# Kernel tuning notes

Measured on AMD Instinct MI355X. Metric: run time of the kernel, lower is better.

Reference implementation:

```python
import jax, jax.numpy as jnp
import numpy as np

DIM = 384
KERNEL = 31
PAD = KERNEL // 2


def setup_inputs() -> dict:
    key = jax.random.key(0)
    k1, k2 = jax.random.split(key)
    x = jax.random.normal(k1, (32, DIM, 56, 56), dtype=jnp.float32)
    weight = jax.random.normal(k2, (DIM, 1, KERNEL, KERNEL), dtype=jnp.float32)
    bias_term = jnp.zeros((DIM,), dtype=jnp.float32)
    return {"x": x, "weight": weight, "bias_term": bias_term}


def reference(x, weight, bias_term):
    # Depthwise conv2d: groups == channels, stride 1, SAME-style padding k//2.
    out = jax.lax.conv_general_dilated(
        x, weight,
        window_strides=(1, 1),
        padding=[(PAD, PAD), (PAD, PAD)],
        dimension_numbers=("NCHW", "OIHW", "NCHW"),
        feature_group_count=DIM,
    )
    return out + bias_term[None, :, None, None]
```

## Files before the change

### kernel.cpp

```cpp
#include <hip/hip_runtime.h>


#define DIMC 384
#define HW 56
#define KS 31
#define PADK 15
#define TROWS 86
#define TCOLS 88
#define RH 14
#define NP 16

typedef _Float16 half2v __attribute__((ext_vector_type(2)));

__device__ __forceinline__ float dot2f(half2v a, half2v b, float c) {
#if defined(__has_builtin) && __has_builtin(__builtin_amdgcn_fdot2)
    return __builtin_amdgcn_fdot2(a, b, c, false);
#else
    return fmaf((float)a.x, (float)b.x, fmaf((float)a.y, (float)b.y, c));
#endif
}

__global__ __launch_bounds__(256, 4)
void dwconv31_dot2(const float* __restrict__ x,
                   const float* __restrict__ w,
                   const float* __restrict__ bias,
                   float* __restrict__ out)
{
    __shared__ _Float16 t0[TROWS * TCOLS];
    __shared__ _Float16 t1[TROWS * TCOLS];
    __shared__ half2v  wlds[KS * NP];

    const int plane = blockIdx.x;
    const int c = plane % DIMC;
    const float* __restrict__ xp = x + (size_t)plane * (HW * HW);
    const float* __restrict__ wp = w + (size_t)c * (KS * KS);
    const int tid = threadIdx.x;

    for (int i = tid; i < KS * NP; i += 256) {
        int kh = i / NP, p = i - kh * NP;
        float a = wp[kh * KS + 2 * p];
        float b = (2 * p + 1 < KS) ? wp[kh * KS + 2 * p + 1] : 0.0f;
        half2v hv;
        hv.x = (_Float16)a;
        hv.y = (_Float16)b;
        wlds[i] = hv;
    }

    for (int idx = tid; idx < TROWS * TCOLS; idx += 256) {
        int r  = idx / TCOLS;
        int cc = idx - r * TCOLS;
        int gr = r - PADK;
        int gc = cc - PADK;
        float v = 0.0f;
        if ((unsigned)gr < (unsigned)HW && (unsigned)gc < (unsigned)HW)
            v = xp[gr * HW + gc];
        _Float16 hv = (_Float16)v;
        t0[r * TCOLS + cc] = hv;
        if (cc >= 1) t1[r * TCOLS + cc - 1] = hv;
        else         t1[r * TCOLS + TCOLS - 1] = (_Float16)0.0f;
    }
    __syncthreads();

    const int tx = tid & 63;
    const int h0 = (tid >> 6) * RH;

    float acc[RH];
#pragma unroll
    for (int j = 0; j < RH; ++j) acc[j] = 0.0f;

    if (tx < HW) {
        const _Float16* base = (tx & 1) ? (t1 + (tx - 1)) : (t0 + tx);

#pragma unroll 1
        for (int p = 0; p < NP; ++p) {
            const _Float16* colp = base + 2 * p;
#pragma unroll 1
            for (int khc = 0; khc < 2; ++khc) {
                const int kh0 = khc * 16;
                const int nkh = khc ? 15 : 16;

                half2v xr[29];
#pragma unroll
                for (int i = 0; i < 29; ++i)
                    xr[i] = *(const half2v*)(colp + (h0 + kh0 + i) * TCOLS);

#pragma unroll
                for (int kk = 0; kk < 16; ++kk) {
                    if (kk < nkh) {
                        half2v wv = wlds[(kh0 + kk) * NP + p];
#pragma unroll
                        for (int j = 0; j < RH; ++j)
                            acc[j] = dot2f(xr[kk + j], wv, acc[j]);
                    }
                }
            }
        }

        const float b = bias[c];
        float* __restrict__ op = out + (size_t)plane * (HW * HW);
#pragma unroll
        for (int j = 0; j < RH; ++j)
            op[(h0 + j) * HW + tx] = acc[j] + b;
    }
}

extern "C" void kernel_launch(void* const* d_in, const int* in_sizes, int n_in,
                              void* d_out, int out_size, void* d_ws, size_t ws_size,
                              hipStream_t stream) {
    const float* x    = (const float*)d_in[0];
    const float* wgt  = (const float*)d_in[1];
    const float* bias = (const float*)d_in[2];
    float* out = (float*)d_out;

    const int nplanes = 32 * DIMC;
    dwconv31_dot2<<<nplanes, 256, 0, stream>>>(x, wgt, bias, out);
}
```

Measured before the change: 908.7 us.

## Transpose LDS tile to column-major and pair vertical taps for dot2

```diff
diff --git a/kernel.cpp b/kernel.cpp
--- a/kernel.cpp
+++ b/kernel.cpp
@@ -1,16 +1,17 @@
 #include <hip/hip_runtime.h>
+#include <stdint.h>
 
 
 #define DIMC 384
 #define HW 56
 #define KS 31
-#define PADK 15
-#define TROWS 86
-#define TCOLS 88
-#define RH 14
-#define NP 16
+#define RH 28
+#define NM 16
+#define TW 86
+#define TH 88
 
 typedef _Float16 half2v __attribute__((ext_vector_type(2)));
+typedef _Float16 half8v __attribute__((ext_vector_type(8)));
 
 __device__ __forceinline__ float dot2f(half2v a, half2v b, float c) {
 #if defined(__has_builtin) && __has_builtin(__builtin_amdgcn_fdot2)
@@ -20,83 +21,100 @@
 #endif
 }
 
-__global__ __launch_bounds__(256, 4)
-void dwconv31_dot2(const float* __restrict__ x,
-                   const float* __restrict__ w,
-                   const float* __restrict__ bias,
-                   float* __restrict__ out)
+template<int G>
+__device__ __forceinline__ void conv_cols(const _Float16* __restrict__ tile,
+                                          const half2v* __restrict__ wlds,
+                                          int tx, float* __restrict__ acc)
 {
-    __shared__ _Float16 t0[TROWS * TCOLS];
-    __shared__ _Float16 t1[TROWS * TCOLS];
-    __shared__ half2v  wlds[KS * NP];
+    constexpr int P0 = 14 * G;
+    constexpr int AG = P0 & ~3;
+    constexpr int DG = P0 - AG;
+
+#pragma unroll 1
+    for (int kw = 0; kw < KS; ++kw) {
+        const int col = tx + kw;
+        const char* cbase = (const char*)tile + col * (TH * 2) + AG * 4;
+
+        half2v X[32];
+#pragma unroll
+        for (int q = 0; q < 8; ++q) {
+            half8v r = *(const half8v*)(cbase + 16 * q);
+            X[4 * q + 0] = __builtin_shufflevector(r, r, 0, 1);
+            X[4 * q + 1] = __builtin_shufflevector(r, r, 2, 3);
+            X[4 * q + 2] = __builtin_shufflevector(r, r, 4, 5);
+            X[4 * q + 3] = __builtin_shufflevector(r, r, 6, 7);
+        }
+
+        half2v Wt[32];
+        const char* wbase = (const char*)wlds + (kw << 7);
+#pragma unroll
+        for (int q = 0; q < 8; ++q) {
+            half8v r = *(const half8v*)(wbase + 16 * q);
+            Wt[4 * q + 0] = __builtin_shufflevector(r, r, 0, 1);
+            Wt[4 * q + 1] = __builtin_shufflevector(r, r, 2, 3);
+            Wt[4 * q + 2] = __builtin_shufflevector(r, r, 4, 5);
+            Wt[4 * q + 3] = __builtin_shufflevector(r, r, 6, 7);
+        }
+
+#pragma unroll
+        for (int j = 0; j < RH; ++j) {
+            const int off = DG + ((j + (j & 1)) >> 1);
+            const int ws  = (j & 1) ? 0 : 16;
+#pragma unroll
+            for (int m = 0; m < NM; ++m)
+                acc[j] = dot2f(X[off + m], Wt[ws + m], acc[j]);
+        }
+    }
+}
+
+__global__ __launch_bounds__(128, 4)
+void dwconv31_v5(const float* __restrict__ x, const float* __restrict__ w,
+                 const float* __restrict__ bias, float* __restrict__ out)
+{
+    __shared__ __align__(16) _Float16 tile[TW * TH];
+    __shared__ __align__(16) half2v  wlds[KS * 32];
 
     const int plane = blockIdx.x;
     const int c = plane % DIMC;
     const float* __restrict__ xp = x + (size_t)plane * (HW * HW);
-    const float* __restrict__ wp = w + (size_t)c * (KS * KS);
+    const float* __restrict__ wc = w + (size_t)c * (KS * KS);
     const int tid = threadIdx.x;
 
-    for (int i = tid; i < KS * NP; i += 256) {
-        int kh = i / NP, p = i - kh * NP;
-        float a = wp[kh * KS + 2 * p];
-        float b = (2 * p + 1 < KS) ? wp[kh * KS + 2 * p + 1] : 0.0f;
-        half2v hv;
-        hv.x = (_Float16)a;
-        hv.y = (_Float16)b;
-        wlds[i] = hv;
+    for (int i = tid; i < KS * NM; i += 128) {
+        int kw = i >> 4, m = i & (NM - 1);
+        float t0 = wc[(2 * m) * KS + kw];
+        float t1 = (2 * m + 1 < KS) ? wc[(2 * m + 1) * KS + kw] : 0.0f;
+        float tm = (m > 0)          ? wc[(2 * m - 1) * KS + kw] : 0.0f;
+        half2v wa; wa.x = (_Float16)t0; wa.y = (_Float16)t1;
+        half2v wb; wb.x = (_Float16)tm; wb.y = (_Float16)t0;
+        wlds[(kw << 5) + m]      = wa;
+        wlds[(kw << 5) + NM + m] = wb;
     }
 
-    for (int idx = tid; idx < TROWS * TCOLS; idx += 256) {
-        int r  = idx / TCOLS;
-        int cc = idx - r * TCOLS;
-        int gr = r - PADK;
-        int gc = cc - PADK;
+    for (int idx = tid; idx < TW * TH; idx += 128) {
+        int hs   = idx / TW;
+        int wcol = idx - hs * TW;
+        int h = hs - 16, gc = wcol - 15;
         float v = 0.0f;
-        if ((unsigned)gr < (unsigned)HW && (unsigned)gc < (unsigned)HW)
-            v = xp[gr * HW + gc];
-        _Float16 hv = (_Float16)v;
-        t0[r * TCOLS + cc] = hv;
-        if (cc >= 1) t1[r * TCOLS + cc - 1] = hv;
-        else         t1[r * TCOLS + TCOLS - 1] = (_Float16)0.0f;
+        if ((unsigned)h < (unsigned)HW && (unsigned)gc < (unsigned)HW)
+            v = xp[h * HW + gc];
+        tile[wcol * TH + hs] = (_Float16)v;
     }
     __syncthreads();
 
     const int tx = tid & 63;
-    const int h0 = (tid >> 6) * RH;
-
-    float acc[RH];
-#pragma unroll
-    for (int j = 0; j < RH; ++j) acc[j] = 0.0f;
+    const int g  = tid >> 6;
 
     if (tx < HW) {
-        const _Float16* base = (tx & 1) ? (t1 + (tx - 1)) : (t0 + tx);
+        float acc[RH];
+#pragma unroll
+        for (int j = 0; j < RH; ++j) acc[j] = 0.0f;
 
-#pragma unroll 1
-        for (int p = 0; p < NP; ++p) {
-            const _Float16* colp = base + 2 * p;
-#pragma unroll 1
-            for (int khc = 0; khc < 2; ++khc) {
-                const int kh0 = khc * 16;
-                const int nkh = khc ? 15 : 16;
-
-                half2v xr[29];
-#pragma unroll
-                for (int i = 0; i < 29; ++i)
-                    xr[i] = *(const half2v*)(colp + (h0 + kh0 + i) * TCOLS);
-
-#pragma unroll
-                for (int kk = 0; kk < 16; ++kk) {
-                    if (kk < nkh) {
-                        half2v wv = wlds[(kh0 + kk) * NP + p];
-#pragma unroll
-                        for (int j = 0; j < RH; ++j)
-                            acc[j] = dot2f(xr[kk + j], wv, acc[j]);
-                    }
-                }
-            }
-        }
+        if (g == 0) conv_cols<0>(tile, wlds, tx, acc);
+        else        conv_cols<1>(tile, wlds, tx, acc);
 
         const float b = bias[c];
+        const int h0 = g * RH;
         float* __restrict__ op = out + (size_t)plane * (HW * HW);
 #pragma unroll
         for (int j = 0; j < RH; ++j)
@@ -113,5 +131,5 @@
     float* out = (float*)d_out;
 
     const int nplanes = 32 * DIMC;
-    dwconv31_dot2<<<nplanes, 256, 0, stream>>>(x, wgt, bias, out);
+    dwconv31_v5<<<nplanes, 128, 0, stream>>>(x, wgt, bias, out);
 }
```

Result: faster. 879.5 us (-3.2%).
